# Performance work log

Hardware: AMD Instinct MI355X
Metric: run time of the kernel (lower is better)

Reference implementation:

```python
import jax, jax.numpy as jnp
import numpy as np

WEIGHT = 0.15  # APPR residual constant (constructor arg `weight`)
N_NODES = 100000
D_FEAT = 64
N_EDGES = 1600000


def setup_inputs() -> dict:
    key = jax.random.key(0)
    kx, ke = jax.random.split(key)
    x = jax.random.normal(kx, (N_NODES, D_FEAT), dtype=jnp.float32)
    edge_index = jax.random.randint(ke, (2, N_EDGES), 0, N_NODES, dtype=jnp.int64)
    return {"x": x, "edge_index": edge_index}


def reference(x, edge_index):
    # PyG flow='source_to_target': message x_j = x[edge_index[0]],
    # scatter-add onto destination nodes edge_index[1].
    src = edge_index[0]
    dst = edge_index[1]
    aggr = jax.ops.segment_sum(x[src], dst, num_segments=x.shape[0])  # [N, D]
    return x + WEIGHT * aggr
```

## Files before the change

kernel.cpp:

```cpp
#include <hip/hip_runtime.h>
#include <hip/hip_bf16.h>

#define APPR_WEIGHT 0.15f
#define D_FEAT 64
#define BUCKET_BITS 7
#define BUCKET_NODES 128
#define MAX_NB 1024
#define SCAT_THREADS 1024
#define SCAT_EPT 16
#define SCAT_EPB (SCAT_THREADS * SCAT_EPT)
#define CSR_BUF 8192
#define BCAP 2560

__global__ void appr_copy_kernel(const float4* __restrict__ x,
                                 float4* __restrict__ out, int n4) {
    int i = blockIdx.x * blockDim.x + threadIdx.x;
    if (i < n4) out[i] = x[i];
}

__global__ void appr_scatter_kernel(const float* __restrict__ x,
                                    const int* __restrict__ src,
                                    const int* __restrict__ dst,
                                    float* __restrict__ out,
                                    int n_edges) {
    long long idx = (long long)blockIdx.x * blockDim.x + threadIdx.x;
    long long total = (long long)n_edges * D_FEAT;
    if (idx >= total) return;
    int e = (int)(idx >> 6);
    int f = (int)(idx & 63);
    float v = APPR_WEIGHT * x[(long long)src[e] * D_FEAT + f];
    unsafeAtomicAdd(&out[(long long)dst[e] * D_FEAT + f], v);
}

__global__ void bucket_scatter_kernel(const int* __restrict__ src,
                                      const int* __restrict__ dst,
                                      int* __restrict__ cursor,
                                      unsigned int* __restrict__ grouped,
                                      int n_edges, int nb) {
    __shared__ int hist[MAX_NB];
    __shared__ int gbase[MAX_NB];
    __shared__ int lcur[MAX_NB];
    int tid = threadIdx.x;
    for (int i = tid; i < nb; i += SCAT_THREADS) { hist[i] = 0; lcur[i] = 0; }
    __syncthreads();

    long long base = (long long)blockIdx.x * SCAT_EPB;
    int mysrc[SCAT_EPT];
    int mydst[SCAT_EPT];
#pragma unroll
    for (int k = 0; k < SCAT_EPT; ++k) {
        long long e = base + (long long)k * SCAT_THREADS + tid;
        if (e < n_edges) {
            mysrc[k] = src[e];
            mydst[k] = dst[e];
            atomicAdd(&hist[mydst[k] >> BUCKET_BITS], 1);
        } else {
            mydst[k] = -1;
        }
    }
    __syncthreads();
    for (int i = tid; i < nb; i += SCAT_THREADS) {
        int c = hist[i];
        gbase[i] = c ? atomicAdd(&cursor[i], c) : 0;
    }
    __syncthreads();
#pragma unroll
    for (int k = 0; k < SCAT_EPT; ++k) {
        if (mydst[k] >= 0) {
            int b = mydst[k] >> BUCKET_BITS;
            int r = atomicAdd(&lcur[b], 1);
            grouped[gbase[b] + r] =
                ((unsigned)mysrc[k] << BUCKET_BITS) |
                (unsigned)(mydst[k] & (BUCKET_NODES - 1));
        }
    }
}


__global__ void convert_bf16_kernel(const float4* __restrict__ x4,
                                    ushort4* __restrict__ xh4, int n4) {
    int i = blockIdx.x * blockDim.x + threadIdx.x;
    if (i >= n4) return;
    float4 v = x4[i];
    ushort4 h;
    __hip_bfloat16 b0 = __float2bfloat16(v.x);
    __hip_bfloat16 b1 = __float2bfloat16(v.y);
    __hip_bfloat16 b2 = __float2bfloat16(v.z);
    __hip_bfloat16 b3 = __float2bfloat16(v.w);
    h.x = *(unsigned short*)&b0;
    h.y = *(unsigned short*)&b1;
    h.z = *(unsigned short*)&b2;
    h.w = *(unsigned short*)&b3;
    xh4[i] = h;
}

__global__ void cursor_init_kernel(int* __restrict__ cursor, int nb) {
    int i = threadIdx.x;
    if (i < nb) cursor[i] = i * BCAP;
}

__global__ void csr_build_fixed_kernel(unsigned int* grouped,
                                       const int* __restrict__ cursor,
                                       int* __restrict__ node_beg,
                                       int* __restrict__ node_end,
                                       int n_nodes) {
    __shared__ unsigned int buf[BCAP];
    __shared__ int hist[BUCKET_NODES];
    __shared__ int excl[BUCKET_NODES];
    __shared__ int cur[BUCKET_NODES];
    int tid = threadIdx.x;
    int b = blockIdx.x;
    int beg = b * BCAP;
    int cnt = cursor[b] - beg;
    if (cnt > BCAP) cnt = BCAP;

    if (tid < BUCKET_NODES) hist[tid] = 0;
    __syncthreads();
    for (int i = tid; i < cnt; i += blockDim.x) {
        unsigned int w = grouped[beg + i];
        buf[i] = w;
        atomicAdd(&hist[w & (BUCKET_NODES - 1)], 1);
    }
    __syncthreads();
    int v = (tid < BUCKET_NODES) ? hist[tid] : 0;
    if (tid < BUCKET_NODES) excl[tid] = v;
    __syncthreads();
    for (int off = 1; off < BUCKET_NODES; off <<= 1) {
        int t = (tid < BUCKET_NODES && tid >= off) ? excl[tid - off] : 0;
        __syncthreads();
        if (tid < BUCKET_NODES) excl[tid] += t;
        __syncthreads();
    }
    if (tid < BUCKET_NODES) {
        int e = excl[tid] - v;
        cur[tid] = e;
        int node = (b << BUCKET_BITS) + tid;
        if (node < n_nodes) {
            node_beg[node] = beg + e;
            node_end[node] = beg + e + v;
        }
    }
    __syncthreads();
    for (int i = tid; i < cnt; i += blockDim.x) {
        unsigned int w = buf[i];
        int pos = atomicAdd(&cur[w & (BUCKET_NODES - 1)], 1);
        grouped[beg + pos] = w >> BUCKET_BITS;
    }
}

__global__ void csr_aggregate_bf16_kernel(const ushort4* __restrict__ xh4,
                                          const float4* __restrict__ x4,
                                          const int* __restrict__ node_beg,
                                          const int* __restrict__ node_end,
                                          const unsigned int* __restrict__ srcs,
                                          float4* __restrict__ out4,
                                          int n_nodes) {
    int gid = blockIdx.x * blockDim.x + threadIdx.x;
    int node = gid >> 5;
    if (node >= n_nodes) return;
    int l32 = threadIdx.x & 31;
    int sub = l32 >> 4;
    int q = l32 & 15;

    int nbeg = node_beg[node];
    int nend = node_end[node];

    float4 acc = make_float4(0.f, 0.f, 0.f, 0.f);
    for (int e0 = nbeg; e0 < nend; e0 += 16) {
#pragma unroll
        for (int u = 0; u < 8; ++u) {
            int i = e0 + u * 2 + sub;
            if (i < nend) {
                int s = (int)srcs[i];
                ushort4 h = xh4[s * 16 + q];
                acc.x += __uint_as_float((unsigned)h.x << 16);
                acc.y += __uint_as_float((unsigned)h.y << 16);
                acc.z += __uint_as_float((unsigned)h.z << 16);
                acc.w += __uint_as_float((unsigned)h.w << 16);
            }
        }
    }
    acc.x += __shfl_xor(acc.x, 16, 64);
    acc.y += __shfl_xor(acc.y, 16, 64);
    acc.z += __shfl_xor(acc.z, 16, 64);
    acc.w += __shfl_xor(acc.w, 16, 64);

    if (sub == 0) {
        float4 xv = x4[node * 16 + q];
        float4 o;
        o.x = xv.x + APPR_WEIGHT * acc.x;
        o.y = xv.y + APPR_WEIGHT * acc.y;
        o.z = xv.z + APPR_WEIGHT * acc.z;
        o.w = xv.w + APPR_WEIGHT * acc.w;
        out4[node * 16 + q] = o;
    }
}


__global__ void bucket_hist_kernel(const int* __restrict__ dst,
                                   int* __restrict__ bcount,
                                   int n_edges, int nb) {
    __shared__ int h[MAX_NB];
    for (int i = threadIdx.x; i < nb; i += blockDim.x) h[i] = 0;
    __syncthreads();
    for (long long e = blockIdx.x * (long long)blockDim.x + threadIdx.x;
         e < n_edges; e += (long long)gridDim.x * blockDim.x) {
        atomicAdd(&h[dst[e] >> BUCKET_BITS], 1);
    }
    __syncthreads();
    for (int i = threadIdx.x; i < nb; i += blockDim.x)
        if (h[i]) atomicAdd(&bcount[i], h[i]);
}

__global__ void bucket_scan_kernel(const int* __restrict__ bcount,
                                   int* __restrict__ boff,
                                   int* __restrict__ cursor, int nb) {
    __shared__ int lds[MAX_NB];
    int tid = threadIdx.x;
    int v = (tid < nb) ? bcount[tid] : 0;
    lds[tid] = v;
    __syncthreads();
    for (int off = 1; off < MAX_NB; off <<= 1) {
        int t = (tid >= off) ? lds[tid - off] : 0;
        __syncthreads();
        lds[tid] += t;
        __syncthreads();
    }
    if (tid < nb) {
        int excl = lds[tid] - v;
        boff[tid] = excl;
        cursor[tid] = excl;
    }
    if (tid == nb - 1) boff[nb] = lds[tid];
}

__global__ void csr_build_kernel(unsigned int* grouped,
                                 const int* __restrict__ boff,
                                 int* __restrict__ node_off,
                                 int n_nodes, int nb) {
    __shared__ unsigned int buf[CSR_BUF];
    __shared__ int hist[BUCKET_NODES];
    __shared__ int excl[BUCKET_NODES];
    __shared__ int cur[BUCKET_NODES];
    int tid = threadIdx.x;
    int b = blockIdx.x;
    int beg = boff[b];
    int end = boff[b + 1];
    int cnt = end - beg;

    if (tid < BUCKET_NODES) hist[tid] = 0;
    __syncthreads();
    for (int i = tid; i < cnt; i += blockDim.x) {
        unsigned int w = grouped[beg + i];
        buf[i] = w;
        atomicAdd(&hist[w & (BUCKET_NODES - 1)], 1);
    }
    __syncthreads();
    int v = (tid < BUCKET_NODES) ? hist[tid] : 0;
    if (tid < BUCKET_NODES) excl[tid] = v;
    __syncthreads();
    for (int off = 1; off < BUCKET_NODES; off <<= 1) {
        int t = (tid < BUCKET_NODES && tid >= off) ? excl[tid - off] : 0;
        __syncthreads();
        if (tid < BUCKET_NODES) excl[tid] += t;
        __syncthreads();
    }
    if (tid < BUCKET_NODES) {
        int e = excl[tid] - v;
        cur[tid] = e;
        int node = (b << BUCKET_BITS) + tid;
        if (node < n_nodes) node_off[node] = beg + e;
    }
    if (b == nb - 1 && tid == 0) node_off[n_nodes] = end;
    __syncthreads();
    for (int i = tid; i < cnt; i += blockDim.x) {
        unsigned int w = buf[i];
        int pos = atomicAdd(&cur[w & (BUCKET_NODES - 1)], 1);
        grouped[beg + pos] = w >> BUCKET_BITS;
    }
}

__global__ void csr_aggregate_kernel(const float4* __restrict__ x4,
                                     const int* __restrict__ node_off,
                                     const unsigned int* __restrict__ srcs,
                                     float4* __restrict__ out4,
                                     int n_nodes) {
    int gid = blockIdx.x * blockDim.x + threadIdx.x;
    int node = gid >> 6;
    if (node >= n_nodes) return;
    int lane = threadIdx.x & 63;
    int sub = lane >> 4;
    int q = lane & 15;

    int nbeg = node_off[node];
    int nend = node_off[node + 1];

    float4 acc = make_float4(0.f, 0.f, 0.f, 0.f);
    for (int e0 = nbeg; e0 < nend; e0 += 16) {
#pragma unroll
        for (int u = 0; u < 4; ++u) {
            int i = e0 + u * 4 + sub;
            if (i < nend) {
                int s = (int)srcs[i];
                float4 vv = x4[s * (D_FEAT / 4) + q];
                acc.x += vv.x; acc.y += vv.y; acc.z += vv.z; acc.w += vv.w;
            }
        }
    }
    acc.x += __shfl_xor(acc.x, 16, 64);
    acc.y += __shfl_xor(acc.y, 16, 64);
    acc.z += __shfl_xor(acc.z, 16, 64);
    acc.w += __shfl_xor(acc.w, 16, 64);
    acc.x += __shfl_xor(acc.x, 32, 64);
    acc.y += __shfl_xor(acc.y, 32, 64);
    acc.z += __shfl_xor(acc.z, 32, 64);
    acc.w += __shfl_xor(acc.w, 32, 64);

    if (lane < 16) {
        float4 xv = x4[node * (D_FEAT / 4) + q];
        float4 o;
        o.x = xv.x + APPR_WEIGHT * acc.x;
        o.y = xv.y + APPR_WEIGHT * acc.y;
        o.z = xv.z + APPR_WEIGHT * acc.z;
        o.w = xv.w + APPR_WEIGHT * acc.w;
        out4[node * (D_FEAT / 4) + q] = o;
    }
}

extern "C" void kernel_launch(void* const* d_in, const int* in_sizes, int n_in,
                              void* d_out, int out_size, void* d_ws, size_t ws_size,
                              hipStream_t stream) {
    const float* x = (const float*)d_in[0];
    const int* edge_index = (const int*)d_in[1];
    float* out = (float*)d_out;

    int n_feat_total = in_sizes[0];
    int n_nodes = n_feat_total / D_FEAT;
    int n_edges = in_sizes[1] / 2;

    const int* src = edge_index;
    const int* dst = edge_index + n_edges;

    int nb = (n_nodes + BUCKET_NODES - 1) >> BUCKET_BITS;
    int sg = (n_edges + SCAT_EPB - 1) / SCAT_EPB;

    size_t need_primary = (size_t)(MAX_NB + 2 * n_nodes + (size_t)nb * BCAP) * 4
                          + (size_t)n_feat_total * 2;
    if (nb <= MAX_NB && n_edges <= nb * BCAP && ws_size >= need_primary) {
        int* cursor           = (int*)d_ws;
        int* node_beg         = cursor + MAX_NB;
        int* node_end         = node_beg + n_nodes;
        unsigned int* grouped = (unsigned int*)(node_end + n_nodes);
        ushort4* xh4          = (ushort4*)(grouped + (size_t)nb * BCAP);

        int n4 = n_feat_total / 4;
        convert_bf16_kernel<<<(n4 + 255) / 256, 256, 0, stream>>>(
            (const float4*)x, xh4, n4);
        cursor_init_kernel<<<1, MAX_NB, 0, stream>>>(cursor, nb);
        bucket_scatter_kernel<<<sg, SCAT_THREADS, 0, stream>>>(
            src, dst, cursor, grouped, n_edges, nb);
        csr_build_fixed_kernel<<<nb, 512, 0, stream>>>(
            grouped, cursor, node_beg, node_end, n_nodes);
        long long threads = (long long)n_nodes * 32;
        csr_aggregate_bf16_kernel<<<(int)((threads + 255) / 256), 256, 0, stream>>>(
            (const ushort4*)xh4, (const float4*)x, node_beg, node_end,
            grouped, (float4*)out, n_nodes);
        return;
    }

    size_t need_r5 = (size_t)(3 * MAX_NB + 1 + n_edges + n_nodes + 1) * sizeof(int);
    if (nb <= MAX_NB && ws_size >= need_r5) {
        int* bcount           = (int*)d_ws;
        int* boff             = bcount + MAX_NB;
        int* cursor           = boff + (MAX_NB + 1);
        unsigned int* grouped = (unsigned int*)(cursor + MAX_NB);
        int* node_off         = (int*)(grouped + n_edges);

        hipMemsetAsync(bcount, 0, (size_t)MAX_NB * sizeof(int), stream);
        bucket_hist_kernel<<<256, 1024, 0, stream>>>(dst, bcount, n_edges, nb);
        bucket_scan_kernel<<<1, MAX_NB, 0, stream>>>(bcount, boff, cursor, nb);
        bucket_scatter_kernel<<<sg, SCAT_THREADS, 0, stream>>>(
            src, dst, cursor, grouped, n_edges, nb);
        csr_build_kernel<<<nb, 512, 0, stream>>>(grouped, boff, node_off,
                                                 n_nodes, nb);
        long long threads = (long long)n_nodes * 64;
        csr_aggregate_kernel<<<(int)((threads + 255) / 256), 256, 0, stream>>>(
            (const float4*)x, node_off, grouped, (float4*)out, n_nodes);
        return;
    }

    int n4 = n_feat_total / 4;
    appr_copy_kernel<<<(n4 + 255) / 256, 256, 0, stream>>>(
        (const float4*)x, (float4*)out, n4);
    long long total = (long long)n_edges * D_FEAT;
    appr_scatter_kernel<<<(int)((total + 255) / 256), 256, 0, stream>>>(
        x, src, dst, out, n_edges);
}
```

Measured before the change: 172.7 us.

## Stage bucketed edges in shared memory for coalesced writes, widen buckets

The bucket scatter kernel now writes each edge into a shared-memory staging buffer ordered by bucket, using a local prefix scan. It then copies each bucket's run to global memory in contiguous wave-wide chunks, replacing the scattered per-edge global writes. Buckets grow to 256 nodes (512 buckets, capacity 5120), edges per thread drop to 8, and the CSR build kernels launch 1024 threads. The cursor-init kernel is folded into the bf16 conversion kernel to save a launch. In exchange the scatter kernel uses much more shared memory (about 32KB staging plus scan arrays), which may reduce occupancy, and the larger buckets increase per-block CSR work.

```diff
diff --git a/kernel.cpp b/kernel.cpp
--- a/kernel.cpp
+++ b/kernel.cpp
@@ -3,14 +3,14 @@
 
 #define APPR_WEIGHT 0.15f
 #define D_FEAT 64
-#define BUCKET_BITS 7
-#define BUCKET_NODES 128
-#define MAX_NB 1024
+#define BUCKET_BITS 8
+#define BUCKET_NODES 256
+#define MAX_NB 512
 #define SCAT_THREADS 1024
-#define SCAT_EPT 16
+#define SCAT_EPT 8
 #define SCAT_EPB (SCAT_THREADS * SCAT_EPT)
 #define CSR_BUF 8192
-#define BCAP 2560
+#define BCAP 5120
 
 __global__ void appr_copy_kernel(const float4* __restrict__ x,
                                  float4* __restrict__ out, int n4) {
@@ -37,7 +37,9 @@
                                       int* __restrict__ cursor,
                                       unsigned int* __restrict__ grouped,
                                       int n_edges, int nb) {
+    __shared__ unsigned int staged[SCAT_EPB];
     __shared__ int hist[MAX_NB];
+    __shared__ int lexcl[MAX_NB];
     __shared__ int gbase[MAX_NB];
     __shared__ int lcur[MAX_NB];
     int tid = threadIdx.x;
@@ -59,26 +61,50 @@
         }
     }
     __syncthreads();
-    for (int i = tid; i < nb; i += SCAT_THREADS) {
-        int c = hist[i];
-        gbase[i] = c ? atomicAdd(&cursor[i], c) : 0;
-    }
-    __syncthreads();
+
+    int hv = (tid < MAX_NB) ? hist[tid] : 0;
+    if (tid < MAX_NB) lexcl[tid] = hv;
+    __syncthreads();
+    for (int off = 1; off < MAX_NB; off <<= 1) {
+        int t = (tid < MAX_NB && tid >= off) ? lexcl[tid - off] : 0;
+        __syncthreads();
+        if (tid < MAX_NB) lexcl[tid] += t;
+        __syncthreads();
+    }
+    if (tid < MAX_NB) lexcl[tid] -= hv;
+    if (tid < nb) gbase[tid] = hv ? atomicAdd(&cursor[tid], hv) : 0;
+    __syncthreads();
+
 #pragma unroll
     for (int k = 0; k < SCAT_EPT; ++k) {
         if (mydst[k] >= 0) {
             int b = mydst[k] >> BUCKET_BITS;
             int r = atomicAdd(&lcur[b], 1);
-            grouped[gbase[b] + r] =
+            staged[lexcl[b] + r] =
                 ((unsigned)mysrc[k] << BUCKET_BITS) |
                 (unsigned)(mydst[k] & (BUCKET_NODES - 1));
         }
     }
+    __syncthreads();
+
+    int wave = tid >> 6;
+    int lane = tid & 63;
+    int nwaves = SCAT_THREADS >> 6;
+    for (int b = wave; b < nb; b += nwaves) {
+        int cnt = hist[b];
+        int lb = lexcl[b];
+        int gb = gbase[b];
+        for (int j = lane; j < cnt; j += 64)
+            grouped[gb + j] = staged[lb + j];
+    }
 }
 
 
 __global__ void convert_bf16_kernel(const float4* __restrict__ x4,
-                                    ushort4* __restrict__ xh4, int n4) {
+                                    ushort4* __restrict__ xh4, int n4,
+                                    int* __restrict__ cursor, int nb) {
+    if (blockIdx.x == 0)
+        for (int b = threadIdx.x; b < nb; b += blockDim.x) cursor[b] = b * BCAP;
     int i = blockIdx.x * blockDim.x + threadIdx.x;
     if (i >= n4) return;
     float4 v = x4[i];
@@ -92,11 +118,6 @@
     h.z = *(unsigned short*)&b2;
     h.w = *(unsigned short*)&b3;
     xh4[i] = h;
-}
-
-__global__ void cursor_init_kernel(int* __restrict__ cursor, int nb) {
-    int i = threadIdx.x;
-    if (i < nb) cursor[i] = i * BCAP;
 }
 
 __global__ void csr_build_fixed_kernel(unsigned int* grouped,
@@ -247,6 +268,7 @@
     int beg = boff[b];
     int end = boff[b + 1];
     int cnt = end - beg;
+    if (cnt > CSR_BUF) cnt = CSR_BUF;
 
     if (tid < BUCKET_NODES) hist[tid] = 0;
     __syncthreads();
@@ -346,7 +368,8 @@
 
     size_t need_primary = (size_t)(MAX_NB + 2 * n_nodes + (size_t)nb * BCAP) * 4
                           + (size_t)n_feat_total * 2;
-    if (nb <= MAX_NB && n_edges <= nb * BCAP && ws_size >= need_primary) {
+    if (nb <= MAX_NB && n_edges <= nb * (BCAP - 16 * (int)sqrtf((float)BCAP))
+        && ws_size >= need_primary) {
         int* cursor           = (int*)d_ws;
         int* node_beg         = cursor + MAX_NB;
         int* node_end         = node_beg + n_nodes;
@@ -355,11 +378,10 @@
 
         int n4 = n_feat_total / 4;
         convert_bf16_kernel<<<(n4 + 255) / 256, 256, 0, stream>>>(
-            (const float4*)x, xh4, n4);
-        cursor_init_kernel<<<1, MAX_NB, 0, stream>>>(cursor, nb);
+            (const float4*)x, xh4, n4, cursor, nb);
         bucket_scatter_kernel<<<sg, SCAT_THREADS, 0, stream>>>(
             src, dst, cursor, grouped, n_edges, nb);
-        csr_build_fixed_kernel<<<nb, 512, 0, stream>>>(
+        csr_build_fixed_kernel<<<nb, 1024, 0, stream>>>(
             grouped, cursor, node_beg, node_end, n_nodes);
         long long threads = (long long)n_nodes * 32;
         csr_aggregate_bf16_kernel<<<(int)((threads + 255) / 256), 256, 0, stream>>>(
@@ -368,8 +390,8 @@
         return;
     }
 
-    size_t need_r5 = (size_t)(3 * MAX_NB + 1 + n_edges + n_nodes + 1) * sizeof(int);
-    if (nb <= MAX_NB && ws_size >= need_r5) {
+    size_t need_dense = (size_t)(3 * MAX_NB + 1 + n_edges + n_nodes + 1) * sizeof(int);
+    if (nb <= MAX_NB && ws_size >= need_dense) {
         int* bcount           = (int*)d_ws;
         int* boff             = bcount + MAX_NB;
         int* cursor           = boff + (MAX_NB + 1);
@@ -381,8 +403,8 @@
         bucket_scan_kernel<<<1, MAX_NB, 0, stream>>>(bcount, boff, cursor, nb);
         bucket_scatter_kernel<<<sg, SCAT_THREADS, 0, stream>>>(
             src, dst, cursor, grouped, n_edges, nb);
-        csr_build_kernel<<<nb, 512, 0, stream>>>(grouped, boff, node_off,
-                                                 n_nodes, nb);
+        csr_build_kernel<<<nb, 1024, 0, stream>>>(grouped, boff, node_off,
+                                                  n_nodes, nb);
         long long threads = (long long)n_nodes * 64;
         csr_aggregate_kernel<<<(int)((threads + 255) / 256), 256, 0, stream>>>(
             (const float4*)x, node_off, grouped, (float4*)out, n_nodes);
```

After: 182.4 us. +5.7%, slower.
